# Performance work log

Hardware: AMD Instinct MI355X
Metric: run time of the kernel (lower is better)

## Reference

```python
import jax, jax.numpy as jnp
import numpy as np

DIST_EPS = 0.1   # distance_eps
NORM_EPS = 0.1   # norm_eps
QUAT_EPS = 1e-3
FA_EPS = 1e-5


def normed_vec(V):
    return V / jnp.sqrt((V ** 2).sum(-1, keepdims=True) + NORM_EPS)


def collect_neighbors(node_h, edge_idx):
    # node_h: (B,N,D), edge_idx: (B,N,K) -> (B,N,K,D)
    B, N, K = edge_idx.shape
    D = node_h.shape[-1]
    idx = jnp.broadcast_to(edge_idx.reshape(B, N * K, 1), (B, N * K, D))
    return jnp.take_along_axis(node_h, idx, axis=1).reshape(B, N, K, D)


def field_average(node_h, C, num_fields):
    # per-field mean, scattered back to residues; residues with C==0 get 0
    onehot = (C[..., None] == (jnp.arange(num_fields) + 1)).astype(node_h.dtype)  # (B,N,F)
    sums = jnp.einsum('bnf,bnd->bfd', onehot, node_h)
    counts = jnp.sum(onehot, axis=1)[..., None]  # (B,F,1)
    avg = sums / (counts + FA_EPS)
    return jnp.einsum('bnf,bfd->bnd', onehot, avg)


def reference_frames(X):
    X_N, X_CA, X_C = X[:, :, 0], X[:, :, 1], X[:, :, 2]
    u_CA_N = normed_vec(X_N - X_CA)
    u_CA_C = normed_vec(X_C - X_CA)
    n_1 = u_CA_N
    n_2 = normed_vec(jnp.cross(n_1, u_CA_C))
    n_3 = normed_vec(jnp.cross(n_1, n_2))
    return jnp.stack([n_1, n_2, n_3], -1)  # (B,N,3,3), frames as columns


def reference_frames_field(X, C, num_fields):
    X_N, X_CA, X_C = X[:, :, 0], X[:, :, 1], X[:, :, 2]
    u_CA_N_avg = field_average(normed_vec(X_N - X_CA), C, num_fields)
    u_CA_C_avg = field_average(normed_vec(X_C - X_CA), C, num_fields)
    n_1 = normed_vec(u_CA_N_avg)
    n_2 = normed_vec(jnp.cross(n_1, normed_vec(u_CA_C_avg)))
    n_3 = normed_vec(jnp.cross(n_1, n_2))
    return jnp.stack([n_1, n_2, n_3], -1)


def quaternions_from_rotations(R):
    Rf = R.reshape(R.shape[:-2] + (9,))
    R00, R01, R02, R10, R11, R12, R20, R21, R22 = [Rf[..., i] for i in range(9)]
    mag = 0.5 * jnp.sqrt(jnp.abs(1.0 + jnp.stack([
        R00 + R11 + R22,
        R00 - R11 - R22,
        -R00 + R11 - R22,
        -R00 - R11 + R22], -1)) + QUAT_EPS)
    signs = jnp.sign(jnp.stack([
        jnp.ones_like(R00), R21 - R12, R02 - R20, R10 - R01], -1))
    q = signs * mag
    return q / jnp.sqrt((q ** 2).sum(-1, keepdims=True))


def transformation_features(X_i, X_j, R_i, R_j):
    dX = X_j - X_i[:, :, None]                    # (B,N,K,3)
    L = jnp.sqrt((dX ** 2).sum(-1, keepdims=True) + DIST_EPS)
    u_ij = jnp.einsum('niab,nija->nijb', R_i, dX / L)
    R_rel = jnp.einsum('niab,nijac->nijbc', R_i, R_j)
    q_ij = quaternions_from_rotations(R_rel)
    return jnp.concatenate([jnp.log(L + DIST_EPS), u_ij, q_ij], -1)  # (B,N,K,8)


def setup_inputs() -> dict:
    key = jax.random.key(0)
    k1, k2, k3 = jax.random.split(key, 3)
    B, N, K, NF = 4, 8192, 48, 16
    X = jax.random.normal(k1, (B, N, 4, 3), dtype=jnp.float32)
    edge_idx = jax.random.randint(k2, (B, N, K), 0, N).astype(jnp.int64)
    C = jax.random.randint(k3, (B, N), 0, NF + 1).astype(jnp.int64)
    return {"X": X, "edge_idx": edge_idx, "C": C, "num_fields": NF}


def reference(X, edge_idx, C, num_fields):
    B, N = X.shape[:2]
    R_i = reference_frames(X)
    R_field_i = reference_frames_field(X, C, num_fields)
    X_i = X[:, :, 1, :]  # CA
    X_j = collect_neighbors(X_i, edge_idx)
    X_field_i = field_average(X_i, C, num_fields)
    X_field_j = collect_neighbors(X_field_i, edge_idx)
    R_field_j = collect_neighbors(R_field_i.reshape(B, N, 9), edge_idx).reshape(B, N, -1, 3, 3)
    R_j = collect_neighbors(R_i.reshape(B, N, 9), edge_idx).reshape(B, N, -1, 3, 3)
    h_ff = transformation_features(X_field_i, X_field_j, R_field_i, R_field_j)
    h_fn = transformation_features(X_field_i, X_j, R_field_i, R_j)
    h_nn = transformation_features(X_i, X_j, R_i, R_j)
    edge_h = jnp.concatenate([h_ff, h_fn, h_nn], -1)  # (B,N,K,24)
    mask_i = (C > 0).astype(edge_h.dtype)[..., None]  # (B,N,1)
    mask_j = collect_neighbors(mask_i, edge_idx)      # (B,N,K,1)
    mask_ij = mask_i[:, :, None] * mask_j
    return mask_ij * edge_h
```

## Files before the change

### kernel.cpp

```cpp
#include <hip/hip_runtime.h>
#include <math.h>

#define NFIELDS 16
#define BATCH   4
#define R64_STRIDE 10

#define DIST_EPS 0.1
#define NORM_EPS 0.1
#define QUAT_EPS 0.001
#define FA_EPS   1e-5

#define TAU_NN 2e-5f
#define TAU_FN 2e-6f

#define FS_THREADS 256
__global__ void prep_pass(const float* __restrict__ X, const int* __restrict__ C,
                          double* __restrict__ Rws64, float* __restrict__ nodeF2,
                          double* __restrict__ accum,
                          int N, int BN, int nodeBlocks) {
    __shared__ double red[FS_THREADS][10];
    int t = threadIdx.x;

    if ((int)blockIdx.x < nodeBlocks) {
        int bn = blockIdx.x * blockDim.x + t;
        if (bn >= BN) return;
        const float* xp = X + (size_t)bn * 12;
        double ax = xp[3], ay = xp[4], az = xp[5];

        double ux = (double)xp[0] - ax, uy = (double)xp[1] - ay, uz = (double)xp[2] - az;
        double r1 = 1.0 / sqrt(ux * ux + uy * uy + uz * uz + NORM_EPS);
        ux *= r1; uy *= r1; uz *= r1;

        double vx = (double)xp[6] - ax, vy = (double)xp[7] - ay, vz = (double)xp[8] - az;
        double r2 = 1.0 / sqrt(vx * vx + vy * vy + vz * vz + NORM_EPS);
        vx *= r2; vy *= r2; vz *= r2;

        double wx = uy * vz - uz * vy, wy = uz * vx - ux * vz, wz = ux * vy - uy * vx;
        double r3 = 1.0 / sqrt(wx * wx + wy * wy + wz * wz + NORM_EPS);
        wx *= r3; wy *= r3; wz *= r3;

        double px = uy * wz - uz * wy, py = uz * wx - ux * wz, pz = ux * wy - uy * wx;
        double r4 = 1.0 / sqrt(px * px + py * py + pz * pz + NORM_EPS);
        px *= r4; py *= r4; pz *= r4;

        double* R = Rws64 + (size_t)bn * R64_STRIDE;
        R[0] = ux; R[1] = uy; R[2] = uz;
        R[3] = wx; R[4] = wy; R[5] = wz;
        R[6] = px; R[7] = py; R[8] = pz;

        int c = C[bn];
        float4* nf = (float4*)(nodeF2 + (size_t)bn * 16);
        nf[0] = make_float4((float)ux, (float)uy, (float)uz, (float)wx);
        nf[1] = make_float4((float)wy, (float)wz, xp[3], xp[4]);
        nf[2] = make_float4(xp[5], (float)c, 0.f, 0.f);
        return;
    }

    int fb = blockIdx.x - nodeBlocks;
    int b  = fb / NFIELDS;
    int f  = fb % NFIELDS + 1;
    const float* Xb = X + (size_t)b * N * 12;
    const int*   Cb = C + (size_t)b * N;

    double s[10];
#pragma unroll
    for (int i = 0; i < 10; i++) s[i] = 0.0;

    for (int n = t; n < N; n += FS_THREADS) {
        if (Cb[n] == f) {
            const float* xp = Xb + (size_t)n * 12;
            double ax = xp[3], ay = xp[4], az = xp[5];
            double ux = (double)xp[0] - ax, uy = (double)xp[1] - ay, uz = (double)xp[2] - az;
            double r1 = 1.0 / sqrt(ux * ux + uy * uy + uz * uz + NORM_EPS);
            double vx = (double)xp[6] - ax, vy = (double)xp[7] - ay, vz = (double)xp[8] - az;
            double r2 = 1.0 / sqrt(vx * vx + vy * vy + vz * vz + NORM_EPS);
            s[0] += ux * r1; s[1] += uy * r1; s[2] += uz * r1;
            s[3] += vx * r2; s[4] += vy * r2; s[5] += vz * r2;
            s[6] += ax;      s[7] += ay;      s[8] += az;
            s[9] += 1.0;
        }
    }

#pragma unroll
    for (int i = 0; i < 10; i++) red[t][i] = s[i];
    __syncthreads();
    for (int off = FS_THREADS / 2; off > 0; off >>= 1) {
        if (t < off) {
#pragma unroll
            for (int i = 0; i < 10; i++) red[t][i] += red[t + off][i];
        }
        __syncthreads();
    }
    if (t < 10) accum[(size_t)fb * 10 + t] = red[0][t];
}

__device__ __forceinline__ double sgn64(double x) {
    return x > 0.0 ? 1.0 : (x < 0.0 ? -1.0 : 0.0);
}

__device__ __forceinline__ void tf64(double xix, double xiy, double xiz,
                                     double xjx, double xjy, double xjz,
                                     const double* __restrict__ Ri,
                                     const double* __restrict__ Rj,
                                     float* __restrict__ o) {
    double dx = xjx - xix, dy = xjy - xiy, dz = xjz - xiz;
    double L = sqrt(dx * dx + dy * dy + dz * dz + DIST_EPS);
    o[0] = (float)log(L + DIST_EPS);
    double il = 1.0 / L;
    double vx = dx * il, vy = dy * il, vz = dz * il;
    o[1] = (float)(Ri[0] * vx + Ri[1] * vy + Ri[2] * vz);
    o[2] = (float)(Ri[3] * vx + Ri[4] * vy + Ri[5] * vz);
    o[3] = (float)(Ri[6] * vx + Ri[7] * vy + Ri[8] * vz);

    double r00 = Ri[0] * Rj[0] + Ri[1] * Rj[1] + Ri[2] * Rj[2];
    double r01 = Ri[0] * Rj[3] + Ri[1] * Rj[4] + Ri[2] * Rj[5];
    double r02 = Ri[0] * Rj[6] + Ri[1] * Rj[7] + Ri[2] * Rj[8];
    double r10 = Ri[3] * Rj[0] + Ri[4] * Rj[1] + Ri[5] * Rj[2];
    double r11 = Ri[3] * Rj[3] + Ri[4] * Rj[4] + Ri[5] * Rj[5];
    double r12 = Ri[3] * Rj[6] + Ri[4] * Rj[7] + Ri[5] * Rj[8];
    double r20 = Ri[6] * Rj[0] + Ri[7] * Rj[1] + Ri[8] * Rj[2];
    double r21 = Ri[6] * Rj[3] + Ri[7] * Rj[4] + Ri[8] * Rj[5];
    double r22 = Ri[6] * Rj[6] + Ri[7] * Rj[7] + Ri[8] * Rj[8];

    double m0 = 0.5 * sqrt(fabs(1.0 + r00 + r11 + r22) + QUAT_EPS);
    double m1 = 0.5 * sqrt(fabs(1.0 + r00 - r11 - r22) + QUAT_EPS);
    double m2 = 0.5 * sqrt(fabs(1.0 - r00 + r11 - r22) + QUAT_EPS);
    double m3 = 0.5 * sqrt(fabs(1.0 - r00 - r11 + r22) + QUAT_EPS);
    double q0 = m0;
    double q1 = sgn64(r21 - r12) * m1;
    double q2 = sgn64(r02 - r20) * m2;
    double q3 = sgn64(r10 - r01) * m3;
    double qn = 1.0 / sqrt(q0 * q0 + q1 * q1 + q2 * q2 + q3 * q3);
    o[4] = (float)(q0 * qn); o[5] = (float)(q1 * qn);
    o[6] = (float)(q2 * qn); o[7] = (float)(q3 * qn);
}

__global__ void field_finish(const double* __restrict__ accum,
                             double* __restrict__ table64,
                             float* __restrict__ tableF,
                             float* __restrict__ hff) {
    int b = blockIdx.x;
    int t = threadIdx.x;

    if (t <= NFIELDS) {
        double* e = table64 + ((size_t)b * (NFIELDS + 1) + t) * 12;
        float*  eF = tableF + ((size_t)b * (NFIELDS + 1) + t) * 12;
        if (t == 0) {
#pragma unroll
            for (int i = 0; i < 12; i++) { e[i] = 0.0; eF[i] = 0.f; }
        } else {
            const double* s = accum + (size_t)(b * NFIELDS + t - 1) * 10;
            double inv = 1.0 / (s[9] + FA_EPS);
            double axv = s[0] * inv, ayv = s[1] * inv, azv = s[2] * inv;
            double bxv = s[3] * inv, byv = s[4] * inv, bzv = s[5] * inv;
            double xx  = s[6] * inv, xy  = s[7] * inv, xz  = s[8] * inv;

            double r1 = 1.0 / sqrt(axv * axv + ayv * ayv + azv * azv + NORM_EPS);
            double n1x = axv * r1, n1y = ayv * r1, n1z = azv * r1;
            double r2 = 1.0 / sqrt(bxv * bxv + byv * byv + bzv * bzv + NORM_EPS);
            bxv *= r2; byv *= r2; bzv *= r2;

            double wx = n1y * bzv - n1z * byv, wy = n1z * bxv - n1x * bzv, wz = n1x * byv - n1y * bxv;
            double r3 = 1.0 / sqrt(wx * wx + wy * wy + wz * wz + NORM_EPS);
            wx *= r3; wy *= r3; wz *= r3;

            double px = n1y * wz - n1z * wy, py = n1z * wx - n1x * wz, pz = n1x * wy - n1y * wx;
            double r4 = 1.0 / sqrt(px * px + py * py + pz * pz + NORM_EPS);
            px *= r4; py *= r4; pz *= r4;

            e[0] = n1x; e[1] = n1y; e[2] = n1z;
            e[3] = wx;  e[4] = wy;  e[5] = wz;
            e[6] = px;  e[7] = py;  e[8] = pz;
            e[9] = xx;  e[10] = xy; e[11] = xz;
#pragma unroll
            for (int i = 0; i < 12; i++) eF[i] = (float)e[i];
        }
    }
    __syncthreads();

    int ci = t >> 4, cj = t & 15;
    const double* fi = table64 + ((size_t)b * (NFIELDS + 1) + ci + 1) * 12;
    const double* fj = table64 + ((size_t)b * (NFIELDS + 1) + cj + 1) * 12;
    float o[8];
    tf64(fi[9], fi[10], fi[11], fj[9], fj[10], fj[11], fi, fj, o);
    float* hp = hff + (((size_t)b * NFIELDS + ci) * NFIELDS + cj) * 8;
    ((float4*)hp)[0] = make_float4(o[0], o[1], o[2], o[3]);
    ((float4*)hp)[1] = make_float4(o[4], o[5], o[6], o[7]);
}

__device__ __forceinline__ void tf32(float xix, float xiy, float xiz,
                                     float xjx, float xjy, float xjz,
                                     const float* __restrict__ Ri,
                                     const float* __restrict__ Rj,
                                     float s1, float s2, float s3,
                                     float* __restrict__ o) {
    float dx = xjx - xix, dy = xjy - xiy, dz = xjz - xiz;
    float L = sqrtf(dx * dx + dy * dy + dz * dz + 0.1f);
    o[0] = logf(L + 0.1f);
    float il = 1.f / L;
    float vx = dx * il, vy = dy * il, vz = dz * il;
    o[1] = Ri[0] * vx + Ri[1] * vy + Ri[2] * vz;
    o[2] = Ri[3] * vx + Ri[4] * vy + Ri[5] * vz;
    o[3] = Ri[6] * vx + Ri[7] * vy + Ri[8] * vz;

    float r00 = Ri[0] * Rj[0] + Ri[1] * Rj[1] + Ri[2] * Rj[2];
    float r11 = Ri[3] * Rj[3] + Ri[4] * Rj[4] + Ri[5] * Rj[5];
    float r22 = Ri[6] * Rj[6] + Ri[7] * Rj[7] + Ri[8] * Rj[8];

    float m0 = 0.5f * sqrtf(fabsf(1.f + r00 + r11 + r22) + 0.001f);
    float m1 = 0.5f * sqrtf(fabsf(1.f + r00 - r11 - r22) + 0.001f);
    float m2 = 0.5f * sqrtf(fabsf(1.f - r00 + r11 - r22) + 0.001f);
    float m3 = 0.5f * sqrtf(fabsf(1.f - r00 - r11 + r22) + 0.001f);
    float q0 = m0;
    float q1 = s1 * m1;
    float q2 = s2 * m2;
    float q3 = s3 * m3;
    float qn = rsqrtf(q0 * q0 + q1 * q1 + q2 * q2 + q3 * q3);
    o[4] = q0 * qn; o[5] = q1 * qn; o[6] = q2 * qn; o[7] = q3 * qn;
}

__device__ __forceinline__ float fsgn(float x) {
    return x > 0.f ? 1.f : (x < 0.f ? -1.f : 0.f);
}
__device__ __forceinline__ float fsgnd(double x) {
    return x > 0.0 ? 1.f : (x < 0.0 ? -1.f : 0.f);
}
__device__ __forceinline__ int hswz(int idx16) {
    return idx16 ^ ((idx16 >> 3) & 7);
}
__device__ __forceinline__ void n3_recompute(const float* __restrict__ r ,
                                             float* __restrict__ n3) {
    float px = r[1] * r[5] - r[2] * r[4];
    float py = r[2] * r[3] - r[0] * r[5];
    float pz = r[0] * r[4] - r[1] * r[3];
    float rr = rsqrtf(px * px + py * py + pz * pz + 0.1f);
    n3[0] = px * rr; n3[1] = py * rr; n3[2] = pz * rr;
}

__device__ __forceinline__ void edge_core(
        const float* __restrict__ rj, const float* __restrict__ cjp,
        const float* __restrict__ ri, const float* __restrict__ cip,
        const float* __restrict__ fF, const float* __restrict__ fp,
        const double* __restrict__ Rws64, const double* __restrict__ table64,
        int b, int bn, int bj, int cn, float* __restrict__ o) {
    float a21 = ri[6]*rj[3] + ri[7]*rj[4] + ri[8]*rj[5] - (ri[3]*rj[6] + ri[4]*rj[7] + ri[5]*rj[8]);
    float a02 = ri[0]*rj[6] + ri[1]*rj[7] + ri[2]*rj[8] - (ri[6]*rj[0] + ri[7]*rj[1] + ri[8]*rj[2]);
    float a10 = ri[3]*rj[0] + ri[4]*rj[1] + ri[5]*rj[2] - (ri[0]*rj[3] + ri[1]*rj[4] + ri[2]*rj[5]);
    float g21 = fF[6]*rj[3] + fF[7]*rj[4] + fF[8]*rj[5] - (fF[3]*rj[6] + fF[4]*rj[7] + fF[5]*rj[8]);
    float g02 = fF[0]*rj[6] + fF[1]*rj[7] + fF[2]*rj[8] - (fF[6]*rj[0] + fF[7]*rj[1] + fF[8]*rj[2]);
    float g10 = fF[3]*rj[0] + fF[4]*rj[1] + fF[5]*rj[2] - (fF[0]*rj[3] + fF[1]*rj[4] + fF[2]*rj[5]);

    float sa21 = fsgn(a21), sa02 = fsgn(a02), sa10 = fsgn(a10);
    float sg21 = fsgn(g21), sg02 = fsgn(g02), sg10 = fsgn(g10);

    float amin = fminf(fminf(fabsf(a21), fabsf(a02)), fabsf(a10));
    float gmin = fminf(fminf(fabsf(g21), fabsf(g02)), fabsf(g10));
    if (amin < TAU_NN || gmin < TAU_FN) {
        const double* RJ = Rws64 + (size_t)bj * R64_STRIDE;
        const double* RI = Rws64 + (size_t)bn * R64_STRIDE;
        const double* FD = table64 + ((size_t)b * (NFIELDS + 1) + cn) * 12;
        double d21 = RI[6]*RJ[3] + RI[7]*RJ[4] + RI[8]*RJ[5] - (RI[3]*RJ[6] + RI[4]*RJ[7] + RI[5]*RJ[8]);
        double d02 = RI[0]*RJ[6] + RI[1]*RJ[7] + RI[2]*RJ[8] - (RI[6]*RJ[0] + RI[7]*RJ[1] + RI[8]*RJ[2]);
        double d10 = RI[3]*RJ[0] + RI[4]*RJ[1] + RI[5]*RJ[2] - (RI[0]*RJ[3] + RI[1]*RJ[4] + RI[2]*RJ[5]);
        double e21 = FD[6]*RJ[3] + FD[7]*RJ[4] + FD[8]*RJ[5] - (FD[3]*RJ[6] + FD[4]*RJ[7] + FD[5]*RJ[8]);
        double e02 = FD[0]*RJ[6] + FD[1]*RJ[7] + FD[2]*RJ[8] - (FD[6]*RJ[0] + FD[7]*RJ[1] + FD[8]*RJ[2]);
        double e10 = FD[3]*RJ[0] + FD[4]*RJ[1] + FD[5]*RJ[2] - (FD[0]*RJ[3] + FD[1]*RJ[4] + FD[2]*RJ[5]);
        sa21 = fsgnd(d21); sa02 = fsgnd(d02); sa10 = fsgnd(d10);
        sg21 = fsgnd(e21); sg02 = fsgnd(e02); sg10 = fsgnd(e10);
    }

    tf32(fp[0], fp[1], fp[2], cjp[0], cjp[1], cjp[2], fF, rj, sg21, sg02, sg10, o + 8);
    tf32(cip[0], cip[1], cip[2], cjp[0], cjp[1], cjp[2], ri, rj, sa21, sa02, sa10, o + 16);
}

template <int KC, int NC>
__global__ __launch_bounds__(256)
void edge_pass_lds(const float* __restrict__ nodeF2, const int* __restrict__ eidx,
                   const float* __restrict__ tableF, const float* __restrict__ hff,
                   const double* __restrict__ Rws64, const double* __restrict__ table64,
                   float* __restrict__ out) {
    __shared__ float4 s_hff[2 * NFIELDS * NFIELDS];
    __shared__ float4 s_tf[(NFIELDS + 1) * 3];
    __shared__ float  s_st[128 * 28];

    const int t   = threadIdx.x;
    const int tid = blockIdx.x * 256 + t;
    const int b   = tid / (KC * NC);
    const int bn  = tid / KC;
    const int bj  = b * NC + eidx[tid];

    {
        const float4* src = (const float4*)(hff + (size_t)b * (NFIELDS * NFIELDS * 8));
        s_hff[hswz(t)]       = src[t];
        s_hff[hswz(t + 256)] = src[t + 256];
        if (t < (NFIELDS + 1) * 3)
            s_tf[t] = ((const float4*)(tableF + (size_t)b * (NFIELDS + 1) * 12))[t];
    }

    const float4* rjp = (const float4*)(nodeF2 + (size_t)bj * 16);
    float4 j0 = rjp[0], j1 = rjp[1], j2 = rjp[2];
    const float4* rip = (const float4*)(nodeF2 + (size_t)bn * 16);
    float4 i0 = rip[0], i1 = rip[1], i2 = rip[2];

    const int cj = (int)j2.y;
    const int cn = (int)i2.y;
    const bool valid = (cn > 0) && (cj > 0);

    float rj[9] = { j0.x, j0.y, j0.z, j0.w, j1.x, j1.y, 0, 0, 0 };
    float cjp[3] = { j1.z, j1.w, j2.x };
    float ri[9] = { i0.x, i0.y, i0.z, i0.w, i1.x, i1.y, 0, 0, 0 };
    float cip[3] = { i1.z, i1.w, i2.x };
    n3_recompute(rj, rj + 6);
    n3_recompute(ri, ri + 6);

    __syncthreads();

    float o[24];
    if (valid) {
        float fF[9], fp[3];
        float4 f0 = s_tf[cn * 3 + 0], f1 = s_tf[cn * 3 + 1], f2 = s_tf[cn * 3 + 2];
        fF[0] = f0.x; fF[1] = f0.y; fF[2] = f0.z; fF[3] = f0.w;
        fF[4] = f1.x; fF[5] = f1.y; fF[6] = f1.z; fF[7] = f1.w;
        fF[8] = f2.x; fp[0] = f2.y; fp[1] = f2.z; fp[2] = f2.w;

        edge_core(rj, cjp, ri, cip, fF, fp, Rws64, table64, b, bn, bj, cn, o);

        int e = ((cn - 1) * NFIELDS + (cj - 1)) * 2;
        float4 h0 = s_hff[hswz(e)];
        float4 h1 = s_hff[hswz(e + 1)];
        o[0] = h0.x; o[1] = h0.y; o[2] = h0.z; o[3] = h0.w;
        o[4] = h1.x; o[5] = h1.y; o[6] = h1.z; o[7] = h1.w;
    } else {
#pragma unroll
        for (int i = 0; i < 24; i++) o[i] = 0.f;
    }

    float4* outv = (float4*)out + (size_t)blockIdx.x * 1536;

    if (t < 128) {
#pragma unroll
        for (int c = 0; c < 6; c++)
            *(float4*)(s_st + t * 28 + c * 4) =
                make_float4(o[4*c], o[4*c+1], o[4*c+2], o[4*c+3]);
    }
    __syncthreads();
#pragma unroll
    for (int r = 0; r < 3; r++) {
        int f  = t + 256 * r;
        int el = f / 6, c = f - el * 6;
        outv[f] = *(const float4*)(s_st + el * 28 + c * 4);
    }
    __syncthreads();
    if (t >= 128) {
#pragma unroll
        for (int c = 0; c < 6; c++)
            *(float4*)(s_st + (t - 128) * 28 + c * 4) =
                make_float4(o[4*c], o[4*c+1], o[4*c+2], o[4*c+3]);
    }
    __syncthreads();
#pragma unroll
    for (int r = 0; r < 3; r++) {
        int f  = 768 + t + 256 * r;
        int fe = f / 6;
        int el = fe - 128, c = f - fe * 6;
        outv[f] = *(const float4*)(s_st + el * 28 + c * 4);
    }
}

__global__ void edge_pass_gen(const float* __restrict__ nodeF2,
                              const int* __restrict__ eidx,
                              const float* __restrict__ tableF,
                              const float* __restrict__ hff,
                              const double* __restrict__ Rws64,
                              const double* __restrict__ table64,
                              float* __restrict__ out,
                              int N, int K, int total) {
    int tid = blockIdx.x * blockDim.x + threadIdx.x;
    if (tid >= total) return;
    int bn = tid / K;
    int b  = bn / N;
    int bj = b * N + eidx[tid];

    const float4* rjp = (const float4*)(nodeF2 + (size_t)bj * 16);
    float4 j0 = rjp[0], j1 = rjp[1], j2 = rjp[2];
    const float4* rip = (const float4*)(nodeF2 + (size_t)bn * 16);
    float4 i0 = rip[0], i1 = rip[1], i2 = rip[2];
    int cj = (int)j2.y;
    int cn = (int)i2.y;

    float o[24];
    if (cn > 0 && cj > 0) {
        float rj[9] = { j0.x, j0.y, j0.z, j0.w, j1.x, j1.y, 0, 0, 0 };
        float cjp[3] = { j1.z, j1.w, j2.x };
        float ri[9] = { i0.x, i0.y, i0.z, i0.w, i1.x, i1.y, 0, 0, 0 };
        float cip[3] = { i1.z, i1.w, i2.x };
        n3_recompute(rj, rj + 6);
        n3_recompute(ri, ri + 6);

        const float4* ftp = (const float4*)(tableF + ((size_t)b * (NFIELDS + 1) + cn) * 12);
        float4 f0 = ftp[0], f1 = ftp[1], f2 = ftp[2];
        float fF[9] = { f0.x, f0.y, f0.z, f0.w, f1.x, f1.y, f1.z, f1.w, f2.x };
        float fp[3] = { f2.y, f2.z, f2.w };

        const float4* hp = (const float4*)(hff +
            (((size_t)b * NFIELDS + (cn - 1)) * NFIELDS + (cj - 1)) * 8);
        float4 h0 = hp[0], h1 = hp[1];
        o[0] = h0.x; o[1] = h0.y; o[2] = h0.z; o[3] = h0.w;
        o[4] = h1.x; o[5] = h1.y; o[6] = h1.z; o[7] = h1.w;
        edge_core(rj, cjp, ri, cip, fF, fp, Rws64, table64, b, bn, bj, cn, o);
    } else {
#pragma unroll
        for (int i = 0; i < 24; i++) o[i] = 0.f;
    }

    float4* op = (float4*)(out + (size_t)tid * 24);
#pragma unroll
    for (int i = 0; i < 6; i++)
        op[i] = make_float4(o[4 * i], o[4 * i + 1], o[4 * i + 2], o[4 * i + 3]);
}

extern "C" void kernel_launch(void* const* d_in, const int* in_sizes, int n_in,
                              void* d_out, int out_size, void* d_ws, size_t ws_size,
                              hipStream_t stream) {
    const float* X  = (const float*)d_in[0];
    const int* eidx = (const int*)d_in[1];
    const int* C    = (const int*)d_in[2];

    const int B  = BATCH;
    const int BN = in_sizes[2];
    const int N  = BN / B;
    const int total = in_sizes[1];
    const int K  = total / BN;

    double* accum   = (double*)d_ws;
    double* table64 = accum + B * NFIELDS * 10;
    double* Rws64   = table64 + B * (NFIELDS + 1) * 12;
    float*  nodeF2  = (float*)(Rws64 + (size_t)BN * R64_STRIDE);
    float*  tableF  = nodeF2 + (size_t)BN * 16;
    float*  hff     = tableF + B * (NFIELDS + 1) * 12;

    int nodeBlocks = (BN + 255) / 256;
    prep_pass<<<nodeBlocks + B * NFIELDS, FS_THREADS, 0, stream>>>(
        X, C, Rws64, nodeF2, accum, N, BN, nodeBlocks);
    field_finish<<<B, 256, 0, stream>>>(accum, table64, tableF, hff);

    if (K == 48 && N == 8192 && (total % 256) == 0) {
        edge_pass_lds<48, 8192><<<total / 256, 256, 0, stream>>>(
            nodeF2, eidx, tableF, hff, Rws64, table64, (float*)d_out);
    } else {
        int eb = (total + 255) / 256;
        edge_pass_gen<<<eb, 256, 0, stream>>>(nodeF2, eidx, tableF, hff,
                                              Rws64, table64, (float*)d_out,
                                              N, K, total);
    }
}
```

Measured before the change: 69.34 us.

## Store third frame axis per node, use fast math, single-pass nontemporal output staging

Prep now writes the third frame vector n3 into the spare node-record slots, so the edge kernels load it instead of recomputing a cross product and rsqrt per endpoint (the specialized kernel still recomputes it for j). tf32 swaps sqrt/div/log for rsqrt and __logf, and the sign function becomes copysignf. The output staging buffer doubles so all 256 threads stage at once, replacing two sync rounds with one, and global writes become nontemporal. The trade-offs are extra shared memory, an extra float4 load per node, and copysignf returning ±1 instead of 0 for exact-zero inputs.

Result: faster. 63.83 us (-8.0%).

```diff
diff --git a/kernel.cpp b/kernel.cpp
--- a/kernel.cpp
+++ b/kernel.cpp
@@ -12,6 +12,8 @@
 
 #define TAU_NN 2e-5f
 #define TAU_FN 2e-6f
+
+typedef float f32x4 __attribute__((ext_vector_type(4)));
 
 #define FS_THREADS 256
 __global__ void prep_pass(const float* __restrict__ X, const int* __restrict__ C,
@@ -52,7 +54,8 @@
         float4* nf = (float4*)(nodeF2 + (size_t)bn * 16);
         nf[0] = make_float4((float)ux, (float)uy, (float)uz, (float)wx);
         nf[1] = make_float4((float)wy, (float)wz, xp[3], xp[4]);
-        nf[2] = make_float4(xp[5], (float)c, 0.f, 0.f);
+        nf[2] = make_float4(xp[5], (float)c, (float)px, (float)py);
+        nf[3] = make_float4((float)pz, 0.f, 0.f, 0.f);
         return;
     }
 
@@ -195,10 +198,11 @@
                                      float s1, float s2, float s3,
                                      float* __restrict__ o) {
     float dx = xjx - xix, dy = xjy - xiy, dz = xjz - xiz;
-    float L = sqrtf(dx * dx + dy * dy + dz * dz + 0.1f);
-    o[0] = logf(L + 0.1f);
-    float il = 1.f / L;
-    float vx = dx * il, vy = dy * il, vz = dz * il;
+    float d2 = dx * dx + dy * dy + dz * dz + 0.1f;
+    float ril = rsqrtf(d2);
+    float L = d2 * ril;
+    o[0] = __logf(L + 0.1f);
+    float vx = dx * ril, vy = dy * ril, vz = dz * ril;
     o[1] = Ri[0] * vx + Ri[1] * vy + Ri[2] * vz;
     o[2] = Ri[3] * vx + Ri[4] * vy + Ri[5] * vz;
     o[3] = Ri[6] * vx + Ri[7] * vy + Ri[8] * vz;
@@ -207,21 +211,18 @@
     float r11 = Ri[3] * Rj[3] + Ri[4] * Rj[4] + Ri[5] * Rj[5];
     float r22 = Ri[6] * Rj[6] + Ri[7] * Rj[7] + Ri[8] * Rj[8];
 
-    float m0 = 0.5f * sqrtf(fabsf(1.f + r00 + r11 + r22) + 0.001f);
-    float m1 = 0.5f * sqrtf(fabsf(1.f + r00 - r11 - r22) + 0.001f);
-    float m2 = 0.5f * sqrtf(fabsf(1.f - r00 + r11 - r22) + 0.001f);
-    float m3 = 0.5f * sqrtf(fabsf(1.f - r00 - r11 + r22) + 0.001f);
-    float q0 = m0;
-    float q1 = s1 * m1;
-    float q2 = s2 * m2;
-    float q3 = s3 * m3;
+    float y0 = fabsf(1.f + r00 + r11 + r22) + 0.001f;
+    float y1 = fabsf(1.f + r00 - r11 - r22) + 0.001f;
+    float y2 = fabsf(1.f - r00 + r11 - r22) + 0.001f;
+    float y3 = fabsf(1.f - r00 - r11 + r22) + 0.001f;
+    float q0 = 0.5f * y0 * rsqrtf(y0);
+    float q1 = s1 * (0.5f * y1 * rsqrtf(y1));
+    float q2 = s2 * (0.5f * y2 * rsqrtf(y2));
+    float q3 = s3 * (0.5f * y3 * rsqrtf(y3));
     float qn = rsqrtf(q0 * q0 + q1 * q1 + q2 * q2 + q3 * q3);
     o[4] = q0 * qn; o[5] = q1 * qn; o[6] = q2 * qn; o[7] = q3 * qn;
 }
 
-__device__ __forceinline__ float fsgn(float x) {
-    return x > 0.f ? 1.f : (x < 0.f ? -1.f : 0.f);
-}
 __device__ __forceinline__ float fsgnd(double x) {
     return x > 0.0 ? 1.f : (x < 0.0 ? -1.f : 0.f);
 }
@@ -250,8 +251,8 @@
     float g02 = fF[0]*rj[6] + fF[1]*rj[7] + fF[2]*rj[8] - (fF[6]*rj[0] + fF[7]*rj[1] + fF[8]*rj[2]);
     float g10 = fF[3]*rj[0] + fF[4]*rj[1] + fF[5]*rj[2] - (fF[0]*rj[3] + fF[1]*rj[4] + fF[2]*rj[5]);
 
-    float sa21 = fsgn(a21), sa02 = fsgn(a02), sa10 = fsgn(a10);
-    float sg21 = fsgn(g21), sg02 = fsgn(g02), sg10 = fsgn(g10);
+    float sa21 = copysignf(1.f, a21), sa02 = copysignf(1.f, a02), sa10 = copysignf(1.f, a10);
+    float sg21 = copysignf(1.f, g21), sg02 = copysignf(1.f, g02), sg10 = copysignf(1.f, g10);
 
     float amin = fminf(fminf(fabsf(a21), fabsf(a02)), fabsf(a10));
     float gmin = fminf(fminf(fabsf(g21), fabsf(g02)), fabsf(g10));
@@ -281,13 +282,18 @@
                    float* __restrict__ out) {
     __shared__ float4 s_hff[2 * NFIELDS * NFIELDS];
     __shared__ float4 s_tf[(NFIELDS + 1) * 3];
-    __shared__ float  s_st[128 * 28];
+    __shared__ float  s_st[256 * 28];
 
     const int t   = threadIdx.x;
+    const int b   = blockIdx.x / ((KC * NC) / 256);
     const int tid = blockIdx.x * 256 + t;
-    const int b   = tid / (KC * NC);
     const int bn  = tid / KC;
     const int bj  = b * NC + eidx[tid];
+
+    const float4* rjp = (const float4*)(nodeF2 + (size_t)bj * 16);
+    float4 j0 = rjp[0], j1 = rjp[1], j2 = rjp[2];
+    const float4* rip = (const float4*)(nodeF2 + (size_t)bn * 16);
+    float4 i0 = rip[0], i1 = rip[1], i2 = rip[2], i3 = rip[3];
 
     {
         const float4* src = (const float4*)(hff + (size_t)b * (NFIELDS * NFIELDS * 8));
@@ -296,27 +302,20 @@
         if (t < (NFIELDS + 1) * 3)
             s_tf[t] = ((const float4*)(tableF + (size_t)b * (NFIELDS + 1) * 12))[t];
     }
-
-    const float4* rjp = (const float4*)(nodeF2 + (size_t)bj * 16);
-    float4 j0 = rjp[0], j1 = rjp[1], j2 = rjp[2];
-    const float4* rip = (const float4*)(nodeF2 + (size_t)bn * 16);
-    float4 i0 = rip[0], i1 = rip[1], i2 = rip[2];
+    __syncthreads();
 
     const int cj = (int)j2.y;
     const int cn = (int)i2.y;
     const bool valid = (cn > 0) && (cj > 0);
 
-    float rj[9] = { j0.x, j0.y, j0.z, j0.w, j1.x, j1.y, 0, 0, 0 };
-    float cjp[3] = { j1.z, j1.w, j2.x };
-    float ri[9] = { i0.x, i0.y, i0.z, i0.w, i1.x, i1.y, 0, 0, 0 };
-    float cip[3] = { i1.z, i1.w, i2.x };
-    n3_recompute(rj, rj + 6);
-    n3_recompute(ri, ri + 6);
-
-    __syncthreads();
-
     float o[24];
     if (valid) {
+        float rj[9] = { j0.x, j0.y, j0.z, j0.w, j1.x, j1.y, 0, 0, 0 };
+        float cjp[3] = { j1.z, j1.w, j2.x };
+        n3_recompute(rj, rj + 6);
+        float ri[9] = { i0.x, i0.y, i0.z, i0.w, i1.x, i1.y, i2.z, i2.w, i3.x };
+        float cip[3] = { i1.z, i1.w, i2.x };
+
         float fF[9], fp[3];
         float4 f0 = s_tf[cn * 3 + 0], f1 = s_tf[cn * 3 + 1], f2 = s_tf[cn * 3 + 2];
         fF[0] = f0.x; fF[1] = f0.y; fF[2] = f0.z; fF[3] = f0.w;
@@ -335,35 +334,19 @@
         for (int i = 0; i < 24; i++) o[i] = 0.f;
     }
 
-    float4* outv = (float4*)out + (size_t)blockIdx.x * 1536;
-
-    if (t < 128) {
-#pragma unroll
-        for (int c = 0; c < 6; c++)
-            *(float4*)(s_st + t * 28 + c * 4) =
-                make_float4(o[4*c], o[4*c+1], o[4*c+2], o[4*c+3]);
-    }
+#pragma unroll
+    for (int c = 0; c < 6; c++)
+        *(float4*)(s_st + t * 28 + c * 4) =
+            make_float4(o[4*c], o[4*c+1], o[4*c+2], o[4*c+3]);
     __syncthreads();
-#pragma unroll
-    for (int r = 0; r < 3; r++) {
+
+    f32x4* outv = (f32x4*)out + (size_t)blockIdx.x * 1536;
+#pragma unroll
+    for (int r = 0; r < 6; r++) {
         int f  = t + 256 * r;
         int el = f / 6, c = f - el * 6;
-        outv[f] = *(const float4*)(s_st + el * 28 + c * 4);
-    }
-    __syncthreads();
-    if (t >= 128) {
-#pragma unroll
-        for (int c = 0; c < 6; c++)
-            *(float4*)(s_st + (t - 128) * 28 + c * 4) =
-                make_float4(o[4*c], o[4*c+1], o[4*c+2], o[4*c+3]);
-    }
-    __syncthreads();
-#pragma unroll
-    for (int r = 0; r < 3; r++) {
-        int f  = 768 + t + 256 * r;
-        int fe = f / 6;
-        int el = fe - 128, c = f - fe * 6;
-        outv[f] = *(const float4*)(s_st + el * 28 + c * 4);
+        f32x4 v = *(const f32x4*)(s_st + el * 28 + c * 4);
+        __builtin_nontemporal_store(v, outv + f);
     }
 }
 
@@ -382,20 +365,18 @@
     int bj = b * N + eidx[tid];
 
     const float4* rjp = (const float4*)(nodeF2 + (size_t)bj * 16);
-    float4 j0 = rjp[0], j1 = rjp[1], j2 = rjp[2];
+    float4 j0 = rjp[0], j1 = rjp[1], j2 = rjp[2], j3 = rjp[3];
     const float4* rip = (const float4*)(nodeF2 + (size_t)bn * 16);
-    float4 i0 = rip[0], i1 = rip[1], i2 = rip[2];
+    float4 i0 = rip[0], i1 = rip[1], i2 = rip[2], i3 = rip[3];
     int cj = (int)j2.y;
     int cn = (int)i2.y;
 
     float o[24];
     if (cn > 0 && cj > 0) {
-        float rj[9] = { j0.x, j0.y, j0.z, j0.w, j1.x, j1.y, 0, 0, 0 };
+        float rj[9] = { j0.x, j0.y, j0.z, j0.w, j1.x, j1.y, j2.z, j2.w, j3.x };
         float cjp[3] = { j1.z, j1.w, j2.x };
-        float ri[9] = { i0.x, i0.y, i0.z, i0.w, i1.x, i1.y, 0, 0, 0 };
+        float ri[9] = { i0.x, i0.y, i0.z, i0.w, i1.x, i1.y, i2.z, i2.w, i3.x };
         float cip[3] = { i1.z, i1.w, i2.x };
-        n3_recompute(rj, rj + 6);
-        n3_recompute(ri, ri + 6);
 
         const float4* ftp = (const float4*)(tableF + ((size_t)b * (NFIELDS + 1) + cn) * 12);
         float4 f0 = ftp[0], f1 = ftp[1], f2 = ftp[2];
```
